# Performance work log

Measured on AMD Instinct MI355X. Metric: run time of the kernel, lower is better.

## Reference

```python
import jax, jax.numpy as jnp
import numpy as np

N_NODES = 50000
N_EDGES = 800000
X_DIM = 32
E_DIM = 32
HID = 64
OUT = 32


def setup_inputs() -> dict:
    key = jax.random.key(0)
    ks = jax.random.split(key, 6)
    x = jax.random.normal(ks[0], (N_NODES, X_DIM), dtype=jnp.float32)
    edge_index = jax.random.randint(ks[1], (2, N_EDGES), 0, N_NODES, dtype=jnp.int64)
    edge_attr = jax.random.normal(ks[2], (N_EDGES, E_DIM), dtype=jnp.float32)
    in_dim = 2 * X_DIM + E_DIM  # 96
    W1 = jax.random.normal(ks[3], (in_dim, HID), dtype=jnp.float32) * (1.0 / np.sqrt(in_dim))
    b1 = jnp.zeros((HID,), dtype=jnp.float32)
    W2 = jax.random.normal(ks[4], (HID, OUT), dtype=jnp.float32) * (1.0 / np.sqrt(HID))
    b2 = jnp.zeros((OUT,), dtype=jnp.float32)
    return {"x": x, "edge_index": edge_index, "edge_attr": edge_attr,
            "W1": W1, "b1": b1, "W2": W2, "b2": b2}


def reference(x, edge_index, edge_attr, W1, b1, W2, b2):
    num_nodes = x.shape[0]
    rol, col = edge_index[0], edge_index[1]
    # gather endpoint features + edge attr -> [E, 2*x_dim + e_dim]
    e_feat = jnp.concatenate([x[rol], x[col], edge_attr], axis=-1)
    # 2-layer MLP (ReLU hidden)
    h = jax.nn.relu(e_feat @ W1 + b1)
    v = h @ W2 + b2  # [E, OUT]
    # scatter-max aggregation into destination nodes (empty segments -> -inf)
    x_cand = jax.ops.segment_max(v, col, num_segments=num_nodes)
    # elementwise max residual against trailing slice of x
    return jnp.maximum(x_cand, x[:, -v.shape[-1]:])
```

## Files before the change

kernel.cpp:

```cpp
#include <hip/hip_runtime.h>


constexpr int XD   = 32;
constexpr int HID  = 64;
constexpr int OUTD = 32;
constexpr int BM   = 128;
constexpr int ASTR = 104;
constexpr int HSTR = 72;
constexpr int BIN_SHIFT = 6;
constexpr int BINW  = 1 << BIN_SHIFT;
constexpr int BLK_E = 8192;
constexpr int EPB   = BLK_E / 256;

typedef __attribute__((ext_vector_type(8)))  short    short8;
typedef __attribute__((ext_vector_type(4)))  float    f32x4;
typedef __attribute__((ext_vector_type(4)))  float    floatx4;

static __device__ __forceinline__ unsigned f2bf(float f) {
    union { float f; unsigned u; } x; x.f = f;
    unsigned r = x.u + 0x7fff + ((x.u >> 16) & 1);
    return r >> 16;
}
static __device__ __forceinline__ unsigned encf(float f) {
    unsigned u = __float_as_uint(f);
    return (u >> 31) ? ~u : (u | 0x80000000u);
}
static __device__ __forceinline__ float decf(unsigned k) {
    return __uint_as_float((k >> 31) ? (k & 0x7fffffffu) : ~k);
}

__global__ __launch_bounds__(256) void prep(
    const float* __restrict__ x, unsigned* __restrict__ xbf,
    const float* __restrict__ W1, const float* __restrict__ W2,
    unsigned* __restrict__ w1s, unsigned* __restrict__ w2s, int total8)
{
    const int i = blockIdx.x * 256 + threadIdx.x;

    if (i < total8) {
        const float4* src = reinterpret_cast<const float4*>(x) + (size_t)i * 2;
        float4 a = src[0], b = src[1];
        uint4 o;
        o.x = f2bf(a.x) | (f2bf(a.y) << 16);
        o.y = f2bf(a.z) | (f2bf(a.w) << 16);
        o.z = f2bf(b.x) | (f2bf(b.y) << 16);
        o.w = f2bf(b.z) | (f2bf(b.w) << 16);
        reinterpret_cast<uint4*>(xbf)[i] = o;
    }

    if (i < 768) {
        const int ti = i >> 6, lane = i & 63;
        const int nt = ti / 3, ks = ti % 3;
        const int col = nt * 16 + (lane & 15);
        const int k0  = ks * 32 + ((lane >> 4) << 3);
        unsigned o[4];
#pragma unroll
        for (int p = 0; p < 4; ++p)
            o[p] = f2bf(W1[(k0 + 2 * p) * HID + col]) |
                   (f2bf(W1[(k0 + 2 * p + 1) * HID + col]) << 16);
        reinterpret_cast<uint4*>(w1s)[i] = make_uint4(o[0], o[1], o[2], o[3]);
    } else if (i < 1024) {
        const int tt = i - 768;
        const int ti = tt >> 6, lane = tt & 63;
        const int nt = ti >> 1, ks = ti & 1;
        const int col = nt * 16 + (lane & 15);
        const int k0  = ks * 32 + ((lane >> 4) << 3);
        unsigned o[4];
#pragma unroll
        for (int p = 0; p < 4; ++p)
            o[p] = f2bf(W2[(k0 + 2 * p) * OUTD + col]) |
                   (f2bf(W2[(k0 + 2 * p + 1) * OUTD + col]) << 16);
        reinterpret_cast<uint4*>(w2s)[tt] = make_uint4(o[0], o[1], o[2], o[3]);
    }
}

__global__ __launch_bounds__(256) void bin_hist(
    const int* __restrict__ ei, unsigned* __restrict__ cnt,
    int n_edges, int nbins)
{
    __shared__ unsigned lh[1024];
    const int t = threadIdx.x;
    for (int i = t; i < nbins; i += 256) lh[i] = 0u;
    __syncthreads();
    const int chunk = blockIdx.x * BLK_E;
#pragma unroll
    for (int i = 0; i < EPB; ++i) {
        const int e = chunk + i * 256 + t;
        if (e < n_edges)
            atomicAdd(&lh[((unsigned)ei[n_edges + e]) >> BIN_SHIFT], 1u);
    }
    __syncthreads();
    for (int i = t; i < nbins; i += 256)
        cnt[(size_t)blockIdx.x * nbins + i] = lh[i];
}

__global__ __launch_bounds__(128) void bin_off(
    const unsigned* __restrict__ cnt, unsigned* __restrict__ off,
    unsigned* __restrict__ totals, int nblk, int nbins)
{
    __shared__ unsigned ts[128];
    const int j = blockIdx.x;
    const int t = threadIdx.x;
    const unsigned d = (t < nblk) ? cnt[(size_t)t * nbins + j] : 0u;
    ts[t] = d;
    __syncthreads();
#pragma unroll
    for (int o = 1; o < 128; o <<= 1) {
        unsigned v = (t >= o) ? ts[t - o] : 0u;
        __syncthreads();
        ts[t] += v;
        __syncthreads();
    }
    if (t < nblk) off[(size_t)t * nbins + j] = ts[t] - d;
    if (t == 127) totals[j] = ts[127];
}

__global__ __launch_bounds__(256) void base_scan(
    const unsigned* __restrict__ totals, unsigned* __restrict__ base, int nbins)
{
    __shared__ unsigned ts[256];
    const int t  = threadIdx.x;
    const int i0 = t * 4;
    unsigned d0 = (i0     < nbins) ? totals[i0]     : 0u;
    unsigned d1 = (i0 + 1 < nbins) ? totals[i0 + 1] : 0u;
    unsigned d2 = (i0 + 2 < nbins) ? totals[i0 + 2] : 0u;
    unsigned d3 = (i0 + 3 < nbins) ? totals[i0 + 3] : 0u;
    ts[t] = d0 + d1 + d2 + d3;
    __syncthreads();
#pragma unroll
    for (int o = 1; o < 256; o <<= 1) {
        unsigned v = (t >= o) ? ts[t - o] : 0u;
        __syncthreads();
        ts[t] += v;
        __syncthreads();
    }
    const unsigned excl = (t == 0) ? 0u : ts[t - 1];
    const unsigned e0 = excl, e1 = e0 + d0, e2 = e1 + d1, e3 = e2 + d2;
    if (i0     < nbins) base[i0]     = e0;
    if (i0 + 1 < nbins) base[i0 + 1] = e1;
    if (i0 + 2 < nbins) base[i0 + 2] = e2;
    if (i0 + 3 < nbins) base[i0 + 3] = e3;
    if (t == 255) base[nbins] = ts[255];
}

__global__ __launch_bounds__(256) void bin_write(
    const int* __restrict__ ei, const unsigned* __restrict__ off,
    const unsigned* __restrict__ base, uint2* __restrict__ rec,
    int n_edges, int nbins)
{
    __shared__ unsigned loff[1024];
    __shared__ unsigned lrank[1024];
    const int t = threadIdx.x;
    const int b = blockIdx.x;
    for (int i = t; i < nbins; i += 256) {
        loff[i]  = base[i] + off[(size_t)b * nbins + i];
        lrank[i] = 0u;
    }
    __syncthreads();
    const int chunk = b * BLK_E;
#pragma unroll
    for (int i = 0; i < EPB; ++i) {
        const int e = chunk + i * 256 + t;
        if (e < n_edges) {
            const unsigned row = (unsigned)ei[e];
            const unsigned col = (unsigned)ei[n_edges + e];
            const unsigned bin = col >> BIN_SHIFT;
            const unsigned r   = atomicAdd(&lrank[bin], 1u);
            rec[loff[bin] + r] = make_uint2((row << 16) | col, (unsigned)e);
        }
    }
}

__global__ __launch_bounds__(256) void edge_mlp_fused(
    const unsigned* __restrict__ xbf,
    const uint2*    __restrict__ rec,
    const float*    __restrict__ ea,
    const unsigned* __restrict__ w1s,
    const unsigned* __restrict__ w2s,
    const float*    __restrict__ b1,
    const float*    __restrict__ b2,
    const float*    __restrict__ x,
    const unsigned* __restrict__ base,
    float*          __restrict__ out,
    int n_edges, int n_nodes)
{
    __shared__ alignas(16) unsigned short Albs[BM * ASTR];
    __shared__ alignas(16) unsigned short Hlds[BM * HSTR];
    __shared__ unsigned accK[BINW * OUTD];
    __shared__ unsigned rcsE[BM];
    __shared__ unsigned rcsR[BM];
    __shared__ unsigned rcsC[BM];

    const int t    = threadIdx.x;
    const int lane = t & 63;
    const int wave = t >> 6;
    const int bin  = blockIdx.x;
    const int n0   = bin << BIN_SHIFT;

    const unsigned sbeg = base[bin];
    const unsigned send = base[bin + 1];

    short8 w1f[12];
#pragma unroll
    for (int ti = 0; ti < 12; ++ti)
        w1f[ti] = *reinterpret_cast<const short8*>(w1s + (size_t)(ti * 64 + lane) * 4);
    short8 w2f[4];
#pragma unroll
    for (int ti = 0; ti < 4; ++ti)
        w2f[ti] = *reinterpret_cast<const short8*>(w2s + (size_t)(ti * 64 + lane) * 4);
    float bb1[4];
#pragma unroll
    for (int nt = 0; nt < 4; ++nt) bb1[nt] = b1[nt * 16 + (lane & 15)];
    float bb2[2];
#pragma unroll
    for (int nt = 0; nt < 2; ++nt) bb2[nt] = b2[nt * 16 + (lane & 15)];

#pragma unroll
    for (int k = 0; k < (BINW * OUTD) / 256; ++k) {
        const int idx = t + k * 256;
        const int g   = n0 + (idx >> 5);
        const float r = (g < n_nodes) ? x[(size_t)g * XD + (idx & 31)] : 0.0f;
        accK[idx] = encf(r);
    }

    const int ntile = (int)(send - sbeg + BM - 1) / BM;
    for (int tile = 0; tile < ntile; ++tile) {
        __syncthreads();

        if (t < BM) {
            unsigned p = sbeg + tile * BM + t;
            if (p >= send) p = send - 1;
            const uint2 q = rec[p];
            rcsE[t] = q.y; rcsR[t] = q.x >> 16; rcsC[t] = q.x & 0xffffu;
        }
        __syncthreads();

        {
            const int m    = t & 127;
            const int side = t >> 7;
            const unsigned id = side ? rcsC[m] : rcsR[m];
            const uint4* src = reinterpret_cast<const uint4*>(xbf + (size_t)id * 16);
#pragma unroll
            for (int q = 0; q < 4; ++q)
                *reinterpret_cast<uint4*>(&Albs[m * ASTR + side * 32 + q * 8]) = src[q];
        }
        {
#pragma unroll
            for (int i = 0; i < 4; ++i) {
                const int f = t + i * 256;
                const int m = f >> 3;
                const int c = (f & 7) * 4;
                const unsigned e = rcsE[m];
                const floatx4 d = __builtin_nontemporal_load(
                    reinterpret_cast<const floatx4*>(ea + (size_t)e * 32 + c));
                uint2 pk;
                pk.x = f2bf(d.x) | (f2bf(d.y) << 16);
                pk.y = f2bf(d.z) | (f2bf(d.w) << 16);
                *reinterpret_cast<uint2*>(&Albs[m * ASTR + 64 + c]) = pk;
            }
        }
        __syncthreads();

        f32x4 acc1[2][4];
#pragma unroll
        for (int mi = 0; mi < 2; ++mi)
#pragma unroll
            for (int nt = 0; nt < 4; ++nt) acc1[mi][nt] = (f32x4){0.f, 0.f, 0.f, 0.f};
#pragma unroll
        for (int ks = 0; ks < 3; ++ks) {
#pragma unroll
            for (int mi = 0; mi < 2; ++mi) {
                const int mt = wave * 2 + mi;
                short8 afrag = *reinterpret_cast<const short8*>(
                    &Albs[(mt * 16 + (lane & 15)) * ASTR + ks * 32 + ((lane >> 4) << 3)]);
#pragma unroll
                for (int nt = 0; nt < 4; ++nt)
                    acc1[mi][nt] = __builtin_amdgcn_mfma_f32_16x16x32_bf16(
                        afrag, w1f[nt * 3 + ks], acc1[mi][nt], 0, 0, 0);
            }
        }

#pragma unroll
        for (int mi = 0; mi < 2; ++mi) {
            const int mt = wave * 2 + mi;
#pragma unroll
            for (int nt = 0; nt < 4; ++nt)
#pragma unroll
                for (int r = 0; r < 4; ++r) {
                    const float h = fmaxf(acc1[mi][nt][r] + bb1[nt], 0.0f);
                    Hlds[(mt * 16 + ((lane >> 4) << 2) + r) * HSTR + nt * 16 + (lane & 15)] =
                        (unsigned short)f2bf(h);
                }
        }
        __syncthreads();

        f32x4 acc2[2][2];
#pragma unroll
        for (int mi = 0; mi < 2; ++mi)
#pragma unroll
            for (int nt = 0; nt < 2; ++nt) acc2[mi][nt] = (f32x4){0.f, 0.f, 0.f, 0.f};
#pragma unroll
        for (int ks = 0; ks < 2; ++ks) {
#pragma unroll
            for (int mi = 0; mi < 2; ++mi) {
                const int mt = wave * 2 + mi;
                short8 hfrag = *reinterpret_cast<const short8*>(
                    &Hlds[(mt * 16 + (lane & 15)) * HSTR + ks * 32 + ((lane >> 4) << 3)]);
#pragma unroll
                for (int nt = 0; nt < 2; ++nt)
                    acc2[mi][nt] = __builtin_amdgcn_mfma_f32_16x16x32_bf16(
                        hfrag, w2f[nt * 2 + ks], acc2[mi][nt], 0, 0, 0);
            }
        }

#pragma unroll
        for (int mi = 0; mi < 2; ++mi) {
            const int mt = wave * 2 + mi;
#pragma unroll
            for (int nt = 0; nt < 2; ++nt)
#pragma unroll
                for (int r = 0; r < 4; ++r) {
                    const int row = mt * 16 + ((lane >> 4) << 2) + r;
                    const float val = acc2[mi][nt][r] + bb2[nt];
                    const int ln = (int)rcsC[row] - n0;
                    atomicMax(&accK[ln * OUTD + nt * 16 + (lane & 15)], encf(val));
                }
        }
    }

    __syncthreads();
#pragma unroll
    for (int k = 0; k < (BINW * OUTD) / 256; ++k) {
        const int idx = t + k * 256;
        const int g   = n0 + (idx >> 5);
        if (g < n_nodes)
            out[(size_t)g * OUTD + (idx & 31)] = decf(accK[idx]);
    }
}

extern "C" void kernel_launch(void* const* d_in, const int* in_sizes, int n_in,
                              void* d_out, int out_size, void* d_ws, size_t ws_size,
                              hipStream_t stream)
{
    const float* x  = (const float*)d_in[0];
    const int*   ei = (const int*)  d_in[1];
    const float* ea = (const float*)d_in[2];
    const float* W1 = (const float*)d_in[3];
    const float* b1 = (const float*)d_in[4];
    const float* W2 = (const float*)d_in[5];
    const float* b2 = (const float*)d_in[6];
    float* out = (float*)d_out;

    const int n_nodes = in_sizes[0] / XD;
    const int n_edges = in_sizes[2] / 32;
    const int nbins   = (n_nodes + BINW - 1) >> BIN_SHIFT;
    const int nblk    = (n_edges + BLK_E - 1) / BLK_E;

    size_t off_b = 0;
    unsigned* cnt    = (unsigned*)((char*)d_ws + off_b); off_b += (size_t)nblk * nbins * 4;
    unsigned* offm   = (unsigned*)((char*)d_ws + off_b); off_b += (size_t)nblk * nbins * 4;
    unsigned* totals = (unsigned*)((char*)d_ws + off_b); off_b += (size_t)nbins * 4;
    unsigned* basep  = (unsigned*)((char*)d_ws + off_b); off_b += (size_t)(nbins + 1) * 4;
    off_b = (off_b + 15) & ~(size_t)15;
    uint2*    rec    = (uint2*)   ((char*)d_ws + off_b); off_b += (size_t)n_edges * 8;
    unsigned* xbf    = (unsigned*)((char*)d_ws + off_b); off_b += (size_t)n_nodes * 16 * 4;
    unsigned* w1s    = (unsigned*)((char*)d_ws + off_b); off_b += 768 * 16;
    unsigned* w2s    = (unsigned*)((char*)d_ws + off_b);

    const int total8 = n_nodes * XD / 8;

    prep<<<(max(total8, 1024) + 255) / 256, 256, 0, stream>>>(x, xbf, W1, W2, w1s, w2s, total8);
    bin_hist<<<nblk, 256, 0, stream>>>(ei, cnt, n_edges, nbins);
    bin_off<<<nbins, 128, 0, stream>>>(cnt, offm, totals, nblk, nbins);
    base_scan<<<1, 256, 0, stream>>>(totals, basep, nbins);
    bin_write<<<nblk, 256, 0, stream>>>(ei, offm, basep, rec, n_edges, nbins);
    edge_mlp_fused<<<nbins, 256, 0, stream>>>(
        xbf, rec, ea, w1s, w2s, b1, b2, x, basep, out, n_edges, n_nodes);
}
```

Before: 104.4 us.

## Halve bin width, alias LDS buffers, fuse histogram into prep kernel

Bins shrink from 64 to 32 nodes, which doubles the number of fused MLP blocks and halves the per-block accumulator LDS. The A and H tiles now share one LDS buffer, with a barrier moved so H overwrites A only after the first MFMA stage, and launch bounds ask for 4 blocks per CU. The histogram kernel is merged into the prep kernel through block-index dispatch, saving one launch, and the base scan now handles 8 bins per thread to cover the larger bin count. The cost is more scatter and scan work plus smaller, more partially filled edge tiles per bin.

```diff
diff --git a/kernel.cpp b/kernel.cpp
--- a/kernel.cpp
+++ b/kernel.cpp
@@ -7,7 +7,7 @@
 constexpr int BM   = 128;
 constexpr int ASTR = 104;
 constexpr int HSTR = 72;
-constexpr int BIN_SHIFT = 6;
+constexpr int BIN_SHIFT = 5;
 constexpr int BINW  = 1 << BIN_SHIFT;
 constexpr int BLK_E = 8192;
 constexpr int EPB   = BLK_E / 256;
@@ -29,21 +29,43 @@
     return __uint_as_float((k >> 31) ? (k & 0x7fffffffu) : ~k);
 }
 
-__global__ __launch_bounds__(256) void prep(
+__global__ __launch_bounds__(256) void prep_hist(
     const float* __restrict__ x, unsigned* __restrict__ xbf,
     const float* __restrict__ W1, const float* __restrict__ W2,
-    unsigned* __restrict__ w1s, unsigned* __restrict__ w2s, int total8)
-{
-    const int i = blockIdx.x * 256 + threadIdx.x;
+    unsigned* __restrict__ w1s, unsigned* __restrict__ w2s,
+    const int* __restrict__ ei, unsigned* __restrict__ cnt,
+    int n_edges, int nbins, int nblk, int total8)
+{
+    __shared__ unsigned lh[2048];
+    const int t = threadIdx.x;
+    const int b = blockIdx.x;
+
+    if (b < nblk) {
+        for (int i = t; i < nbins; i += 256) lh[i] = 0u;
+        __syncthreads();
+        const int chunk = b * BLK_E;
+#pragma unroll
+        for (int i = 0; i < EPB; ++i) {
+            const int e = chunk + i * 256 + t;
+            if (e < n_edges)
+                atomicAdd(&lh[((unsigned)ei[n_edges + e]) >> BIN_SHIFT], 1u);
+        }
+        __syncthreads();
+        for (int i = t; i < nbins; i += 256)
+            cnt[(size_t)b * nbins + i] = lh[i];
+        return;
+    }
+
+    const int i = (b - nblk) * 256 + t;
 
     if (i < total8) {
         const float4* src = reinterpret_cast<const float4*>(x) + (size_t)i * 2;
-        float4 a = src[0], b = src[1];
+        float4 a = src[0], bb = src[1];
         uint4 o;
-        o.x = f2bf(a.x) | (f2bf(a.y) << 16);
-        o.y = f2bf(a.z) | (f2bf(a.w) << 16);
-        o.z = f2bf(b.x) | (f2bf(b.y) << 16);
-        o.w = f2bf(b.z) | (f2bf(b.w) << 16);
+        o.x = f2bf(a.x)  | (f2bf(a.y)  << 16);
+        o.y = f2bf(a.z)  | (f2bf(a.w)  << 16);
+        o.z = f2bf(bb.x) | (f2bf(bb.y) << 16);
+        o.w = f2bf(bb.z) | (f2bf(bb.w) << 16);
         reinterpret_cast<uint4*>(xbf)[i] = o;
     }
 
@@ -73,26 +95,6 @@
     }
 }
 
-__global__ __launch_bounds__(256) void bin_hist(
-    const int* __restrict__ ei, unsigned* __restrict__ cnt,
-    int n_edges, int nbins)
-{
-    __shared__ unsigned lh[1024];
-    const int t = threadIdx.x;
-    for (int i = t; i < nbins; i += 256) lh[i] = 0u;
-    __syncthreads();
-    const int chunk = blockIdx.x * BLK_E;
-#pragma unroll
-    for (int i = 0; i < EPB; ++i) {
-        const int e = chunk + i * 256 + t;
-        if (e < n_edges)
-            atomicAdd(&lh[((unsigned)ei[n_edges + e]) >> BIN_SHIFT], 1u);
-    }
-    __syncthreads();
-    for (int i = t; i < nbins; i += 256)
-        cnt[(size_t)blockIdx.x * nbins + i] = lh[i];
-}
-
 __global__ __launch_bounds__(128) void bin_off(
     const unsigned* __restrict__ cnt, unsigned* __restrict__ off,
     unsigned* __restrict__ totals, int nblk, int nbins)
@@ -118,13 +120,16 @@
     const unsigned* __restrict__ totals, unsigned* __restrict__ base, int nbins)
 {
     __shared__ unsigned ts[256];
-    const int t  = threadIdx.x;
-    const int i0 = t * 4;
-    unsigned d0 = (i0     < nbins) ? totals[i0]     : 0u;
-    unsigned d1 = (i0 + 1 < nbins) ? totals[i0 + 1] : 0u;
-    unsigned d2 = (i0 + 2 < nbins) ? totals[i0 + 2] : 0u;
-    unsigned d3 = (i0 + 3 < nbins) ? totals[i0 + 3] : 0u;
-    ts[t] = d0 + d1 + d2 + d3;
+    const int t = threadIdx.x;
+    unsigned d[8];
+    unsigned s = 0;
+#pragma unroll
+    for (int k = 0; k < 8; ++k) {
+        const int i = t * 8 + k;
+        d[k] = (i < nbins) ? totals[i] : 0u;
+        s += d[k];
+    }
+    ts[t] = s;
     __syncthreads();
 #pragma unroll
     for (int o = 1; o < 256; o <<= 1) {
@@ -133,13 +138,14 @@
         ts[t] += v;
         __syncthreads();
     }
-    const unsigned excl = (t == 0) ? 0u : ts[t - 1];
-    const unsigned e0 = excl, e1 = e0 + d0, e2 = e1 + d1, e3 = e2 + d2;
-    if (i0     < nbins) base[i0]     = e0;
-    if (i0 + 1 < nbins) base[i0 + 1] = e1;
-    if (i0 + 2 < nbins) base[i0 + 2] = e2;
-    if (i0 + 3 < nbins) base[i0 + 3] = e3;
-    if (t == 255) base[nbins] = ts[255];
+    unsigned run = (t == 0) ? 0u : ts[t - 1];
+#pragma unroll
+    for (int k = 0; k < 8; ++k) {
+        const int i = t * 8 + k;
+        if (i < nbins) base[i] = run;
+        run += d[k];
+    }
+    if (t == 255) base[nbins] = run;
 }
 
 __global__ __launch_bounds__(256) void bin_write(
@@ -147,8 +153,8 @@
     const unsigned* __restrict__ base, uint2* __restrict__ rec,
     int n_edges, int nbins)
 {
-    __shared__ unsigned loff[1024];
-    __shared__ unsigned lrank[1024];
+    __shared__ unsigned loff[2048];
+    __shared__ unsigned lrank[2048];
     const int t = threadIdx.x;
     const int b = blockIdx.x;
     for (int i = t; i < nbins; i += 256) {
@@ -170,7 +176,7 @@
     }
 }
 
-__global__ __launch_bounds__(256) void edge_mlp_fused(
+__global__ __launch_bounds__(256, 4) void edge_mlp_fused(
     const unsigned* __restrict__ xbf,
     const uint2*    __restrict__ rec,
     const float*    __restrict__ ea,
@@ -183,8 +189,7 @@
     float*          __restrict__ out,
     int n_edges, int n_nodes)
 {
-    __shared__ alignas(16) unsigned short Albs[BM * ASTR];
-    __shared__ alignas(16) unsigned short Hlds[BM * HSTR];
+    __shared__ alignas(16) unsigned short S[BM * ASTR];
     __shared__ unsigned accK[BINW * OUTD];
     __shared__ unsigned rcsE[BM];
     __shared__ unsigned rcsR[BM];
@@ -241,7 +246,7 @@
             const uint4* src = reinterpret_cast<const uint4*>(xbf + (size_t)id * 16);
 #pragma unroll
             for (int q = 0; q < 4; ++q)
-                *reinterpret_cast<uint4*>(&Albs[m * ASTR + side * 32 + q * 8]) = src[q];
+                *reinterpret_cast<uint4*>(&S[m * ASTR + side * 32 + q * 8]) = src[q];
         }
         {
 #pragma unroll
@@ -255,7 +260,7 @@
                 uint2 pk;
                 pk.x = f2bf(d.x) | (f2bf(d.y) << 16);
                 pk.y = f2bf(d.z) | (f2bf(d.w) << 16);
-                *reinterpret_cast<uint2*>(&Albs[m * ASTR + 64 + c]) = pk;
+                *reinterpret_cast<uint2*>(&S[m * ASTR + 64 + c]) = pk;
             }
         }
         __syncthreads();
@@ -271,13 +276,14 @@
             for (int mi = 0; mi < 2; ++mi) {
                 const int mt = wave * 2 + mi;
                 short8 afrag = *reinterpret_cast<const short8*>(
-                    &Albs[(mt * 16 + (lane & 15)) * ASTR + ks * 32 + ((lane >> 4) << 3)]);
+                    &S[(mt * 16 + (lane & 15)) * ASTR + ks * 32 + ((lane >> 4) << 3)]);
 #pragma unroll
                 for (int nt = 0; nt < 4; ++nt)
                     acc1[mi][nt] = __builtin_amdgcn_mfma_f32_16x16x32_bf16(
                         afrag, w1f[nt * 3 + ks], acc1[mi][nt], 0, 0, 0);
             }
         }
+        __syncthreads();
 
 #pragma unroll
         for (int mi = 0; mi < 2; ++mi) {
@@ -287,11 +293,10 @@
 #pragma unroll
                 for (int r = 0; r < 4; ++r) {
                     const float h = fmaxf(acc1[mi][nt][r] + bb1[nt], 0.0f);
-                    Hlds[(mt * 16 + ((lane >> 4) << 2) + r) * HSTR + nt * 16 + (lane & 15)] =
+                    S[(mt * 16 + ((lane >> 4) << 2) + r) * HSTR + nt * 16 + (lane & 15)] =
                         (unsigned short)f2bf(h);
                 }
         }
-        __syncthreads();
 
         f32x4 acc2[2][2];
 #pragma unroll
@@ -304,7 +309,7 @@
             for (int mi = 0; mi < 2; ++mi) {
                 const int mt = wave * 2 + mi;
                 short8 hfrag = *reinterpret_cast<const short8*>(
-                    &Hlds[(mt * 16 + (lane & 15)) * HSTR + ks * 32 + ((lane >> 4) << 3)]);
+                    &S[(mt * 16 + (lane & 15)) * HSTR + ks * 32 + ((lane >> 4) << 3)]);
 #pragma unroll
                 for (int nt = 0; nt < 2; ++nt)
                     acc2[mi][nt] = __builtin_amdgcn_mfma_f32_16x16x32_bf16(
@@ -366,10 +371,11 @@
     unsigned* w1s    = (unsigned*)((char*)d_ws + off_b); off_b += 768 * 16;
     unsigned* w2s    = (unsigned*)((char*)d_ws + off_b);
 
-    const int total8 = n_nodes * XD / 8;
-
-    prep<<<(max(total8, 1024) + 255) / 256, 256, 0, stream>>>(x, xbf, W1, W2, w1s, w2s, total8);
-    bin_hist<<<nblk, 256, 0, stream>>>(ei, cnt, n_edges, nbins);
+    const int total8     = n_nodes * XD / 8;
+    const int prep_blk   = (max(total8, 1024) + 255) / 256;
+
+    prep_hist<<<nblk + prep_blk, 256, 0, stream>>>(
+        x, xbf, W1, W2, w1s, w2s, ei, cnt, n_edges, nbins, nblk, total8);
     bin_off<<<nbins, 128, 0, stream>>>(cnt, offm, totals, nblk, nbins);
     base_scan<<<1, 256, 0, stream>>>(totals, basep, nbins);
     bin_write<<<nblk, 256, 0, stream>>>(ei, offm, basep, rec, n_edges, nbins);
```

Result: slower. 143.7 us (+37.7%).
